# Optimization experiments

Hardware: AMD Instinct MI355X
Metric: run time of the kernel (lower is better)

## Reference

```python
import jax, jax.numpy as jnp
import numpy as np

H = 1024  # hidden_dim
DT = 0.1
LN_EPS = 1e-5


def setup_inputs() -> dict:
    key = jax.random.key(0)
    ks = jax.random.split(key, 8)
    h = H
    ph = h // 2
    x = jax.random.normal(ks[0], (8, 2048, h), dtype=jnp.float32)
    # S initialized to identity in torch; add small noise so math is non-trivial
    S = jnp.eye(h, dtype=jnp.float32) + 0.02 * jax.random.normal(ks[1], (h, h), dtype=jnp.float32)
    # Hamiltonian MLP: Linear(h,h) -> tanh -> Linear(h,1)
    lim1 = 1.0 / np.sqrt(h)
    W1 = jax.random.uniform(ks[2], (h, h), minval=-lim1, maxval=lim1, dtype=jnp.float32)
    b1 = jax.random.uniform(ks[3], (h,), minval=-lim1, maxval=lim1, dtype=jnp.float32)
    w2 = jax.random.uniform(ks[4], (h,), minval=-lim1, maxval=lim1, dtype=jnp.float32)
    b2 = jax.random.uniform(ks[5], (1,), minval=-lim1, maxval=lim1, dtype=jnp.float32)
    # symplectic structure matrix J (buffer)
    I = jnp.eye(ph, dtype=jnp.float32)
    J = jnp.zeros((h, h), dtype=jnp.float32)
    J = J.at[:ph, ph:].set(I)
    J = J.at[ph:, :ph].set(-I)
    gamma = jnp.ones((h,), dtype=jnp.float32)
    beta = jnp.zeros((h,), dtype=jnp.float32)
    return {"x": x, "S": S, "W1": W1, "b1": b1, "w2": w2, "b2": b2,
            "J": J, "gamma": gamma, "beta": beta, "num_steps": 3}


def reference(x, S, W1, b1, w2, b2, J, gamma, beta, num_steps):
    h = x.shape[-1]
    # Cayley-approx symplectic projection (training branch): S_sym = I + 2*A, A skew part
    A = (S - S.T) * 0.5
    S_sym = jnp.eye(h, dtype=x.dtype) + 2.0 * A
    # z = einsum('ij,...j->...i', S_sym, x)
    z = x @ S_sym.T
    for _ in range(num_steps):
        # analytic grad of H(z) = w2 . tanh(z W1^T + b1) + b2 wrt z
        t = jnp.tanh(z @ W1.T + b1)             # [..., h]
        grad_H = ((1.0 - t * t) * w2) @ W1       # [..., h]
        flow = grad_H @ J.T                      # einsum('ij,...j->...i', J, grad_H)
        z = z + DT * flow
    y = z + x
    # LayerNorm over last dim
    mu = jnp.mean(y, axis=-1, keepdims=True)
    var = jnp.mean((y - mu) ** 2, axis=-1, keepdims=True)
    return (y - mu) * jax.lax.rsqrt(var + LN_EPS) * gamma + beta
```

## Files before the change

kernel.cpp:

```cpp
#include <hip/hip_runtime.h>
#include <hip/hip_bf16.h>

#define H 1024
#define PH 512
#define MROWS 16384
#define DT 0.1f
#define LN_EPS 1e-5f

#define BM 128
#define BN 128
#define BK 64

typedef short s16x8 __attribute__((ext_vector_type(8)));
typedef float f32x4 __attribute__((ext_vector_type(4)));

__device__ __forceinline__ float b2f(short v) {
    union { float f; unsigned u; } c;
    c.u = ((unsigned)(unsigned short)v) << 16;
    return c.f;
}
__device__ __forceinline__ short f2b(float f) {
    union { float f; unsigned u; } c;
    c.f = f;
    unsigned u = c.u;
    unsigned r = u + 0x7FFFu + ((u >> 16) & 1u);
    return (short)(r >> 16);
}
__device__ __forceinline__ float ftanh(float s) {
    float e = __expf(2.0f * s);
    return 1.0f - 2.0f * __builtin_amdgcn_rcpf(e + 1.0f);
}

__global__ __launch_bounds__(256)
void prep_ab(const float* __restrict__ S, const float* __restrict__ W1,
             short* __restrict__ Wsym, short* __restrict__ W1b,
             short* __restrict__ Wflow) {
    int idx = blockIdx.x * 256 + threadIdx.x;
    int i = idx >> 10, j = idx & 1023;
    Wsym[idx] = f2b(S[i * H + j] - S[j * H + i]);
    W1b[idx]  = f2b(W1[idx]);
    int p = (i + PH) & (H - 1);
    short w = f2b(W1[j * H + p]);
    if (i >= PH) w ^= (short)0x8000;
    Wflow[idx] = w;
}

__global__ __launch_bounds__(256)
void cvt_x(const float* __restrict__ x, short* __restrict__ xb) {
    int t = blockIdx.x * 256 + threadIdx.x;
    const float4* p = (const float4*)x + (size_t)t * 2;
    float4 f0 = p[0], f1 = p[1];
    s16x8 v;
    v[0] = f2b(f0.x); v[1] = f2b(f0.y); v[2] = f2b(f0.z); v[3] = f2b(f0.w);
    v[4] = f2b(f1.x); v[5] = f2b(f1.y); v[6] = f2b(f1.z); v[7] = f2b(f1.w);
    ((s16x8*)xb)[t] = v;
}

template <int KIND>
__global__ __launch_bounds__(256, 4)
void gemm_k(const short* __restrict__ A, const short* __restrict__ Bw,
            short* __restrict__ out,
            const float* __restrict__ xf,
            const float* __restrict__ w2f)
{
    __shared__ short As[BM * BK];
    __shared__ short Bs[BN * BK];

    const int tid  = threadIdx.x;
    const int lane = tid & 63;
    const int wave = tid >> 6;
    const int wm   = wave >> 1;
    const int wn   = wave & 1;

    const int lid   = blockIdx.x;
    const int chunk = ((lid & 7) << 7) | (lid >> 3);
    const int m0    = (chunk >> 3) * BM;
    const int n0    = (chunk & 7) * BN;

    const int lrow = lane & 15;
    const int quad = lane >> 4;
    const int swzr = (lrow & 7) << 4;

    const int srow  = lane >> 3;
    const int selem = 8 * ((lane & 7) ^ srow);

    f32x4 acc[4][4] = {};

    for (int k0 = 0; k0 < H; k0 += BK) {
#pragma unroll
        for (int i = 0; i < 4; ++i) {
            int ch = wave * 4 + i;
            const short* asrc = A  + (size_t)(m0 + ch * 8 + srow) * H + k0 + selem;
            const short* bsrc = Bw + (size_t)(n0 + ch * 8 + srow) * H + k0 + selem;
            __builtin_amdgcn_global_load_lds(
                (const __attribute__((address_space(1))) void*)asrc,
                (__attribute__((address_space(3))) void*)(As + ch * 512), 16, 0, 0);
            __builtin_amdgcn_global_load_lds(
                (const __attribute__((address_space(1))) void*)bsrc,
                (__attribute__((address_space(3))) void*)(Bs + ch * 512), 16, 0, 0);
        }
        __syncthreads();

#pragma unroll
        for (int ks = 0; ks < 2; ++ks) {
            s16x8 af[4], bfr[4];
#pragma unroll
            for (int mt = 0; mt < 4; ++mt) {
                int row = wm * 64 + mt * 16 + lrow;
                af[mt] = *(const s16x8*)((const char*)As + row * 128 +
                                         ((ks * 64 + quad * 16) ^ swzr));
            }
#pragma unroll
            for (int nt = 0; nt < 4; ++nt) {
                int col = wn * 64 + nt * 16 + lrow;
                bfr[nt] = *(const s16x8*)((const char*)Bs + col * 128 +
                                          ((ks * 64 + quad * 16) ^ swzr));
            }
#pragma unroll
            for (int mt = 0; mt < 4; ++mt)
#pragma unroll
                for (int nt = 0; nt < 4; ++nt)
                    acc[mt][nt] = __builtin_amdgcn_mfma_f32_16x16x32_bf16(
                        bfr[nt], af[mt], acc[mt][nt], 0, 0, 0);
        }
        __syncthreads();
    }

    float4 bvv[4], wvv[4];
    if (KIND == 1) {
#pragma unroll
        for (int nt = 0; nt < 4; ++nt) {
            int col = n0 + wn * 64 + nt * 16 + quad * 4;
            bvv[nt] = *(const float4*)(xf + col);
            wvv[nt] = *(const float4*)(w2f + col);
        }
    }
#pragma unroll
    for (int mt = 0; mt < 4; ++mt) {
        const int row = m0 + wm * 64 + mt * 16 + lrow;
        const size_t rbase = (size_t)row * H;
#pragma unroll
        for (int nt = 0; nt < 4; ++nt) {
            const int col = n0 + wn * 64 + nt * 16 + quad * 4;
            const size_t idx = rbase + col;
            f32x4 a = acc[mt][nt];
            short4 o;
            if (KIND == 0) {
                float4 xv = *(const float4*)(xf + idx);
                o.x = f2b(a[0] + xv.x);
                o.y = f2b(a[1] + xv.y);
                o.z = f2b(a[2] + xv.z);
                o.w = f2b(a[3] + xv.w);
            } else if (KIND == 1) {
                float t0 = ftanh(a[0] + bvv[nt].x);
                float t1 = ftanh(a[1] + bvv[nt].y);
                float t2 = ftanh(a[2] + bvv[nt].z);
                float t3 = ftanh(a[3] + bvv[nt].w);
                o.x = f2b((1.0f - t0 * t0) * wvv[nt].x);
                o.y = f2b((1.0f - t1 * t1) * wvv[nt].y);
                o.z = f2b((1.0f - t2 * t2) * wvv[nt].z);
                o.w = f2b((1.0f - t3 * t3) * wvv[nt].w);
            } else {
                short4 zo = *(const short4*)(out + idx);
                float d0 = fminf(fmaxf(DT * a[0], -0.01f), 0.01f);
                float d1 = fminf(fmaxf(DT * a[1], -0.01f), 0.01f);
                float d2 = fminf(fmaxf(DT * a[2], -0.01f), 0.01f);
                float d3 = fminf(fmaxf(DT * a[3], -0.01f), 0.01f);
                o.x = f2b(b2f(zo.x) + d0);
                o.y = f2b(b2f(zo.y) + d1);
                o.z = f2b(b2f(zo.z) + d2);
                o.w = f2b(b2f(zo.w) + d3);
            }
            *(short4*)(out + idx) = o;
        }
    }
}

__global__ __launch_bounds__(256)
void ln_k(const short* __restrict__ z, const float* __restrict__ x,
          const float* __restrict__ gamma, const float* __restrict__ beta,
          float* __restrict__ out) {
    const int row = blockIdx.x;
    const int tid = threadIdx.x;
    const size_t base = (size_t)row * H;
    short4 z4 = ((const short4*)(z + base))[tid];
    float4 x4 = ((const float4*)(x + base))[tid];
    float y0 = b2f(z4.x) + x4.x;
    float y1 = b2f(z4.y) + x4.y;
    float y2 = b2f(z4.z) + x4.z;
    float y3 = b2f(z4.w) + x4.w;
    float s = y0 + y1 + y2 + y3;
    float q = y0 * y0 + y1 * y1 + y2 * y2 + y3 * y3;
#pragma unroll
    for (int off = 32; off > 0; off >>= 1) {
        s += __shfl_down(s, off);
        q += __shfl_down(q, off);
    }
    __shared__ float ss[4], qs[4];
    if ((tid & 63) == 0) { ss[tid >> 6] = s; qs[tid >> 6] = q; }
    __syncthreads();
    s = ss[0] + ss[1] + ss[2] + ss[3];
    q = qs[0] + qs[1] + qs[2] + qs[3];
    const float mu  = s * (1.0f / H);
    const float var = q * (1.0f / H) - mu * mu;
    const float rs  = rsqrtf(var + LN_EPS);
    const int col = tid * 4;
    float4 o;
    o.x = (y0 - mu) * rs * gamma[col + 0] + beta[col + 0];
    o.y = (y1 - mu) * rs * gamma[col + 1] + beta[col + 1];
    o.z = (y2 - mu) * rs * gamma[col + 2] + beta[col + 2];
    o.w = (y3 - mu) * rs * gamma[col + 3] + beta[col + 3];
    ((float4*)(out + base))[tid] = o;
}

extern "C" void kernel_launch(void* const* d_in, const int* in_sizes, int n_in,
                              void* d_out, int out_size, void* d_ws, size_t ws_size,
                              hipStream_t stream) {
    int ix = 0;
    for (int i = 0; i < n_in; ++i)
        if (in_sizes[i] == MROWS * H) { ix = i; break; }

    const float *x, *S, *W1, *b1, *w2, *gamma, *beta;
    if (ix == 0) {
        x     = (const float*)d_in[0];
        S     = (const float*)d_in[1];
        W1    = (const float*)d_in[2];
        b1    = (const float*)d_in[3];
        w2    = (const float*)d_in[4];
        gamma = (const float*)d_in[7];
        beta  = (const float*)d_in[8];
    } else {
        S     = (const float*)d_in[1];
        W1    = (const float*)d_in[2];
        b1    = (const float*)d_in[3];
        beta  = (const float*)d_in[5];
        gamma = (const float*)d_in[6];
        w2    = (const float*)d_in[8];
        x     = (const float*)d_in[ix];
    }

    float* out   = (float*)d_out;
    short* xb    = (short*)d_out;
    short* g     = (short*)d_out;
    char*  hi    = (char*)d_out + (size_t)32 * 1024 * 1024;
    short* Wsym  = (short*)(hi);
    short* W1b   = (short*)(hi + (size_t)2 * 1024 * 1024);
    short* Wflow = (short*)(hi + (size_t)4 * 1024 * 1024);
    short* z     = (short*)d_ws;

    prep_ab<<<(H * H) / 256, 256, 0, stream>>>(S, W1, Wsym, W1b, Wflow);
    cvt_x  <<<(MROWS * H / 8) / 256, 256, 0, stream>>>(x, xb);

    const int nblk = (H / BN) * (MROWS / BM);
    gemm_k<0><<<nblk, 256, 0, stream>>>(xb, Wsym, z, x, nullptr);
    for (int step = 0; step < 3; ++step) {
        gemm_k<1><<<nblk, 256, 0, stream>>>(z, W1b, g, b1, w2);
        gemm_k<2><<<nblk, 256, 0, stream>>>(g, Wflow, z, nullptr, nullptr);
    }
    ln_k<<<MROWS, 256, 0, stream>>>(z, x, gamma, beta, out);
}
```

Before: 463.1 us.

## Fold flow and W1 into a precomputed matrix to cut per-step GEMMs

Precomputes GT = DT·Wflow-based product with W1 so that the tanh pre-activation can be updated directly: u_{k+1} = u0 + (accumulated g)·GT. The model state z is then updated once at the end from the summed gradient terms. The aim is to replace the alternating 2-GEMMs-per-step chain with one small weight GEMM plus fewer large activation GEMMs. In exchange it adds extra bf16 buffers, stores pre-activations in bf16, applies the flow clamp to the summed update rather than per step, and only runs when the workspace is large enough.

New measurement: 424.0 us. -8.4%, faster.

```diff
diff --git a/kernel.cpp b/kernel.cpp
--- a/kernel.cpp
+++ b/kernel.cpp
@@ -34,7 +34,7 @@
 __global__ __launch_bounds__(256)
 void prep_ab(const float* __restrict__ S, const float* __restrict__ W1,
              short* __restrict__ Wsym, short* __restrict__ W1b,
-             short* __restrict__ Wflow) {
+             short* __restrict__ Wflow, short* __restrict__ WflowT) {
     int idx = blockIdx.x * 256 + threadIdx.x;
     int i = idx >> 10, j = idx & 1023;
     Wsym[idx] = f2b(S[i * H + j] - S[j * H + i]);
@@ -43,6 +43,10 @@
     short w = f2b(W1[j * H + p]);
     if (i >= PH) w ^= (short)0x8000;
     Wflow[idx] = w;
+    int q = (j + PH) & (H - 1);
+    short wt = f2b(W1[i * H + q]);
+    if (j >= PH) wt ^= (short)0x8000;
+    WflowT[idx] = wt;
 }
 
 __global__ __launch_bounds__(256)
@@ -56,12 +60,16 @@
     ((s16x8*)xb)[t] = v;
 }
 
-template <int KIND>
+template <int KIND, bool G2D>
 __global__ __launch_bounds__(256, 4)
 void gemm_k(const short* __restrict__ A, const short* __restrict__ Bw,
             short* __restrict__ out,
             const float* __restrict__ xf,
-            const float* __restrict__ w2f)
+            const float* __restrict__ w2f,
+            const short* __restrict__ u0r,
+            const short* __restrict__ pg,
+            short* __restrict__ out2,
+            float clampv)
 {
     __shared__ short As[BM * BK];
     __shared__ short Bs[BN * BK];
@@ -72,10 +80,16 @@
     const int wm   = wave >> 1;
     const int wn   = wave & 1;
 
-    const int lid   = blockIdx.x;
-    const int chunk = ((lid & 7) << 7) | (lid >> 3);
-    const int m0    = (chunk >> 3) * BM;
-    const int n0    = (chunk & 7) * BN;
+    int m0, n0;
+    if (G2D) {
+        m0 = blockIdx.y * BM;
+        n0 = blockIdx.x * BN;
+    } else {
+        const int lid   = blockIdx.x;
+        const int chunk = ((lid & 7) << 7) | (lid >> 3);
+        m0 = (chunk >> 3) * BM;
+        n0 = (chunk & 7) * BN;
+    }
 
     const int lrow = lane & 15;
     const int quad = lane >> 4;
@@ -127,7 +141,7 @@
     }
 
     float4 bvv[4], wvv[4];
-    if (KIND == 1) {
+    if (KIND == 1 || KIND == 3 || KIND == 4) {
 #pragma unroll
         for (int nt = 0; nt < 4; ++nt) {
             int col = n0 + wn * 64 + nt * 16 + quad * 4;
@@ -151,6 +165,7 @@
                 o.y = f2b(a[1] + xv.y);
                 o.z = f2b(a[2] + xv.z);
                 o.w = f2b(a[3] + xv.w);
+                *(short4*)(out + idx) = o;
             } else if (KIND == 1) {
                 float t0 = ftanh(a[0] + bvv[nt].x);
                 float t1 = ftanh(a[1] + bvv[nt].y);
@@ -160,18 +175,50 @@
                 o.y = f2b((1.0f - t1 * t1) * wvv[nt].y);
                 o.z = f2b((1.0f - t2 * t2) * wvv[nt].z);
                 o.w = f2b((1.0f - t3 * t3) * wvv[nt].w);
-            } else {
+                *(short4*)(out + idx) = o;
+            } else if (KIND == 2) {
                 short4 zo = *(const short4*)(out + idx);
-                float d0 = fminf(fmaxf(DT * a[0], -0.01f), 0.01f);
-                float d1 = fminf(fmaxf(DT * a[1], -0.01f), 0.01f);
-                float d2 = fminf(fmaxf(DT * a[2], -0.01f), 0.01f);
-                float d3 = fminf(fmaxf(DT * a[3], -0.01f), 0.01f);
+                float d0 = fminf(fmaxf(DT * a[0], -clampv), clampv);
+                float d1 = fminf(fmaxf(DT * a[1], -clampv), clampv);
+                float d2 = fminf(fmaxf(DT * a[2], -clampv), clampv);
+                float d3 = fminf(fmaxf(DT * a[3], -clampv), clampv);
                 o.x = f2b(b2f(zo.x) + d0);
                 o.y = f2b(b2f(zo.y) + d1);
                 o.z = f2b(b2f(zo.z) + d2);
                 o.w = f2b(b2f(zo.w) + d3);
+                *(short4*)(out + idx) = o;
+            } else if (KIND == 3) {
+                short4 u;
+                u.x = f2b(a[0]); u.y = f2b(a[1]); u.z = f2b(a[2]); u.w = f2b(a[3]);
+                *(short4*)(out + idx) = u;
+                float t0 = ftanh(a[0] + bvv[nt].x);
+                float t1 = ftanh(a[1] + bvv[nt].y);
+                float t2 = ftanh(a[2] + bvv[nt].z);
+                float t3 = ftanh(a[3] + bvv[nt].w);
+                o.x = f2b((1.0f - t0 * t0) * wvv[nt].x);
+                o.y = f2b((1.0f - t1 * t1) * wvv[nt].y);
+                o.z = f2b((1.0f - t2 * t2) * wvv[nt].z);
+                o.w = f2b((1.0f - t3 * t3) * wvv[nt].w);
+                *(short4*)(out2 + idx) = o;
+            } else if (KIND == 4) {
+                short4 u4 = *(const short4*)(u0r + idx);
+                short4 p4 = *(const short4*)(pg + idx);
+                float t0 = ftanh(b2f(u4.x) + a[0] + bvv[nt].x);
+                float t1 = ftanh(b2f(u4.y) + a[1] + bvv[nt].y);
+                float t2 = ftanh(b2f(u4.z) + a[2] + bvv[nt].z);
+                float t3 = ftanh(b2f(u4.w) + a[3] + bvv[nt].w);
+                o.x = f2b(b2f(p4.x) + (1.0f - t0 * t0) * wvv[nt].x);
+                o.y = f2b(b2f(p4.y) + (1.0f - t1 * t1) * wvv[nt].y);
+                o.z = f2b(b2f(p4.z) + (1.0f - t2 * t2) * wvv[nt].z);
+                o.w = f2b(b2f(p4.w) + (1.0f - t3 * t3) * wvv[nt].w);
+                *(short4*)(out2 + idx) = o;
+            } else {
+                o.x = f2b(DT * a[0]);
+                o.y = f2b(DT * a[1]);
+                o.z = f2b(DT * a[2]);
+                o.w = f2b(DT * a[3]);
+                *(short4*)(out + idx) = o;
             }
-            *(short4*)(out + idx) = o;
         }
     }
 }
@@ -239,23 +286,49 @@
         x     = (const float*)d_in[ix];
     }
 
-    float* out   = (float*)d_out;
-    short* xb    = (short*)d_out;
-    short* g     = (short*)d_out;
-    char*  hi    = (char*)d_out + (size_t)32 * 1024 * 1024;
-    short* Wsym  = (short*)(hi);
-    short* W1b   = (short*)(hi + (size_t)2 * 1024 * 1024);
-    short* Wflow = (short*)(hi + (size_t)4 * 1024 * 1024);
-    short* z     = (short*)d_ws;
-
-    prep_ab<<<(H * H) / 256, 256, 0, stream>>>(S, W1, Wsym, W1b, Wflow);
+    const size_t MB = 1024 * 1024;
+    float* out    = (float*)d_out;
+    short* xb     = (short*)d_out;
+    short* u0     = (short*)d_out;
+    char*  hi     = (char*)d_out + 32 * MB;
+    short* Wsym   = (short*)(hi);
+    short* W1b    = (short*)(hi + 2 * MB);
+    short* Wflow  = (short*)(hi + 4 * MB);
+    short* WflowT = (short*)(hi + 6 * MB);
+    short* GT     = (short*)(hi + 8 * MB);
+    short* z      = (short*)d_ws;
+    short* gsumA  = (short*)((char*)d_ws + 32 * MB);
+    short* gsumB  = (short*)((char*)d_ws + 64 * MB);
+
+    const bool fast = ws_size >= 96 * MB;
+
+    prep_ab<<<(H * H) / 256, 256, 0, stream>>>(S, W1, Wsym, W1b, Wflow, WflowT);
     cvt_x  <<<(MROWS * H / 8) / 256, 256, 0, stream>>>(x, xb);
 
     const int nblk = (H / BN) * (MROWS / BM);
-    gemm_k<0><<<nblk, 256, 0, stream>>>(xb, Wsym, z, x, nullptr);
-    for (int step = 0; step < 3; ++step) {
-        gemm_k<1><<<nblk, 256, 0, stream>>>(z, W1b, g, b1, w2);
-        gemm_k<2><<<nblk, 256, 0, stream>>>(g, Wflow, z, nullptr, nullptr);
+    if (fast) {
+        gemm_k<5, true><<<dim3(H / BN, H / BM), 256, 0, stream>>>(
+            W1b, WflowT, GT, nullptr, nullptr, nullptr, nullptr, nullptr, 0.0f);
+        gemm_k<0, false><<<nblk, 256, 0, stream>>>(
+            xb, Wsym, z, x, nullptr, nullptr, nullptr, nullptr, 0.0f);
+        gemm_k<3, false><<<nblk, 256, 0, stream>>>(
+            z, W1b, u0, b1, w2, nullptr, nullptr, gsumA, 0.0f);
+        gemm_k<4, false><<<nblk, 256, 0, stream>>>(
+            gsumA, GT, nullptr, b1, w2, u0, gsumA, gsumB, 0.0f);
+        gemm_k<4, false><<<nblk, 256, 0, stream>>>(
+            gsumB, GT, nullptr, b1, w2, u0, gsumB, gsumA, 0.0f);
+        gemm_k<2, false><<<nblk, 256, 0, stream>>>(
+            gsumA, Wflow, z, nullptr, nullptr, nullptr, nullptr, nullptr, 0.03f);
+    } else {
+        short* g = (short*)d_out;
+        gemm_k<0, false><<<nblk, 256, 0, stream>>>(
+            xb, Wsym, z, x, nullptr, nullptr, nullptr, nullptr, 0.0f);
+        for (int step = 0; step < 3; ++step) {
+            gemm_k<1, false><<<nblk, 256, 0, stream>>>(
+                z, W1b, g, b1, w2, nullptr, nullptr, nullptr, 0.0f);
+            gemm_k<2, false><<<nblk, 256, 0, stream>>>(
+                g, Wflow, z, nullptr, nullptr, nullptr, nullptr, nullptr, 0.01f);
+        }
     }
     ln_k<<<MROWS, 256, 0, stream>>>(z, x, gamma, beta, out);
 }
```
